# Optimization experiments

Measured on AMD Instinct MI355X. Metric: run time of the kernel, lower is better.

Reference implementation:

```python
import jax, jax.numpy as jnp
import numpy as np

NUM_ITERS = 10
G_KSIZE, G_SIGMA = 5, 0.5
BIL_KSIZE, BIL_SIG_COLOR, BIL_SIG_SPACE = 5, 0.5, 5.0
EDGE_KSIZE, EDGE_SIG_COLOR, EDGE_SIG_SPACE = 5, 0.5, 5.0


def _gauss1d(ksize, sigma):
    x = jnp.arange(ksize, dtype=jnp.float32) - ksize // 2  # odd ksize -> centered (kornia)
    g = jnp.exp(-(x * x) / (2.0 * sigma * sigma))
    return g / g.sum()


def gaussian_blur(q, ksize, sigma):
    # separable gaussian blur with reflect padding, kornia GaussianBlur2d semantics
    k = _gauss1d(ksize, sigma)
    r = ksize // 2
    B, C, H, W = q.shape
    qp = jnp.pad(q, ((0, 0), (0, 0), (r, r), (0, 0)), mode='reflect')
    q = sum(k[i] * qp[:, :, i:i + H, :] for i in range(ksize))
    qp = jnp.pad(q, ((0, 0), (0, 0), (0, 0), (r, r)), mode='reflect')
    q = sum(k[i] * qp[:, :, :, i:i + W] for i in range(ksize))
    return q


def bilateral_weights(guide, ksize, sigma_color, sigma_space):
    # kornia joint_bilateral_blur weights (l1 color distance, reflect border).
    # guide: [B, Cg, H, W] -> weights [B, K*K, H, W]; guidance is constant across
    # CRF iterations so we precompute the kernel once.
    B, Cg, H, W = guide.shape
    r = ksize // 2
    g1 = _gauss1d(ksize, sigma_space)
    space = jnp.outer(g1, g1)  # normalized 2d gaussian (kornia get_gaussian_kernel2d)
    gp = jnp.pad(guide, ((0, 0), (0, 0), (r, r), (r, r)), mode='reflect')
    inv2sc2 = -0.5 / (sigma_color * sigma_color)
    ws = []
    for dy in range(ksize):
        for dx in range(ksize):
            d = jnp.abs(gp[:, :, dy:dy + H, dx:dx + W] - guide).sum(axis=1)  # [B,H,W]
            ws.append(space[dy, dx] * jnp.exp(inv2sc2 * d * d))
    return jnp.stack(ws, axis=1)  # [B, K*K, H, W]


def bilateral_apply(q, weights, ksize):
    # q: [B,C,H,W], weights: [B,K*K,H,W]
    B, C, H, W = q.shape
    r = ksize // 2
    qp = jnp.pad(q, ((0, 0), (0, 0), (r, r), (r, r)), mode='reflect')
    num = jnp.zeros_like(q)
    idx = 0
    for dy in range(ksize):
        for dx in range(ksize):
            num = num + weights[:, idx][:, None] * qp[:, :, dy:dy + H, dx:dx + W]
            idx += 1
    den = weights.sum(axis=1)[:, None]  # [B,1,H,W]
    return num / den


def _compat(f):
    # compat matrix is -1 off-diagonal, 0 on diagonal:
    # pairwise[c] = -sum_{c'!=c} f[c'] = f[c] - sum_{c'} f[c']
    return f - f.sum(axis=1, keepdims=True)


def setup_inputs() -> dict:
    key = jax.random.key(0)
    k1, k2, k3 = jax.random.split(key, 3)
    B, C, H, W = 2, 21, 512, 512
    unary_logits = jax.random.normal(k1, (B, C, H, W), dtype=jnp.float32)
    image = jax.random.uniform(k2, (B, 3, H, W), dtype=jnp.float32)
    edges = jax.random.uniform(k3, (B, H, W), dtype=jnp.float32)
    return {"unary_logits": unary_logits, "image": image, "edges": edges}


def reference(unary_logits, image, edges):
    edges4 = edges[:, None]  # [B,1,H,W]
    w_rgb = bilateral_weights(image, BIL_KSIZE, BIL_SIG_COLOR, BIL_SIG_SPACE)
    w_edge = bilateral_weights(edges4, EDGE_KSIZE, EDGE_SIG_COLOR, EDGE_SIG_SPACE)
    q = jax.nn.softmax(unary_logits, axis=1)
    for _ in range(NUM_ITERS):
        sf = gaussian_blur(q, G_KSIZE, G_SIGMA)
        rf = bilateral_apply(q, w_rgb, BIL_KSIZE)
        ef = bilateral_apply(q, w_edge, EDGE_KSIZE)
        pairwise = _compat(sf) + _compat(rf) + _compat(ef)
        q = jax.nn.softmax(unary_logits - pairwise, axis=1)
    return q
```

## Files before the change

### kernel.cpp

```cpp
#include <hip/hip_runtime.h>
#include <math.h>

#define BATCH 2
#define NCH 21
#define CPAD 24
#define HH 512
#define WW 512
#define KS 5
#define RAD 2
#define NTAPS 25
#define NPAIR 13
#define NUM_ITERS 10

#define TX 32
#define TY 8
#define HX (TX + 2*RAD)
#define HY (TY + 2*RAD)
#define HPX (HX * HY)

typedef _Float16 f16;
typedef _Float16 half8 __attribute__((ext_vector_type(8)));
typedef _Float16 half2v __attribute__((ext_vector_type(2)));

__device__ __forceinline__ int refl(int i, int n) {
    if (i < 0) i = -i;
    if (i >= n) i = 2*n - 2 - i;
    return i;
}

__global__ __launch_bounds__(256) void weights_kernel(const float* __restrict__ image,
                                                      const float* __restrict__ edges,
                                                      half2v* __restrict__ wc2) {
    __shared__ float sr_[HY][HX];
    __shared__ float sg_[HY][HX];
    __shared__ float sb_[HY][HX];
    __shared__ float se_[HY][HX];

    const int tx = threadIdx.x;
    const int ty = threadIdx.y;
    const int tid = ty * TX + tx;
    const int x0 = blockIdx.x * TX;
    const int y0 = blockIdx.y * TY;
    const int b = blockIdx.z;
    const int x = x0 + tx;
    const int y = y0 + ty;
    const size_t plane = (size_t)HH * WW;
    const float* img = image + (size_t)b * 3 * plane;
    const float* edg = edges + (size_t)b * plane;

    for (int i = tid; i < HPX; i += TX * TY) {
        int ly = i / HX, lx = i - ly * HX;
        int gy = refl(y0 + ly - RAD, HH);
        int gx = refl(x0 + lx - RAD, WW);
        int g = gy * WW + gx;
        sr_[ly][lx] = img[g];
        sg_[ly][lx] = img[plane + g];
        sb_[ly][lx] = img[2 * plane + g];
        se_[ly][lx] = edg[g];
    }
    __syncthreads();

    float gs[3];
    gs[0] = 1.0f; gs[1] = __expf(-1.0f / 50.0f); gs[2] = __expf(-4.0f / 50.0f);
    float gb[3];
    gb[0] = 1.0f; gb[1] = __expf(-2.0f); gb[2] = __expf(-8.0f);
    float gbs = gb[0] + 2.0f * (gb[1] + gb[2]);
    gb[0] /= gbs; gb[1] /= gbs; gb[2] /= gbs;

    const float r0 = sr_[ty + RAD][tx + RAD];
    const float g0 = sg_[ty + RAD][tx + RAD];
    const float b0 = sb_[ty + RAD][tx + RAD];
    const float e0 = se_[ty + RAD][tx + RAD];

    float wr[NTAPS], we[NTAPS];
    float sr = 0.f, se = 0.f;
#pragma unroll
    for (int dy = 0; dy < KS; dy++) {
#pragma unroll
        for (int dx = 0; dx < KS; dx++) {
            float sp = gs[abs(dy - RAD)] * gs[abs(dx - RAD)];
            float d = fabsf(sr_[ty + dy][tx + dx] - r0)
                    + fabsf(sg_[ty + dy][tx + dx] - g0)
                    + fabsf(sb_[ty + dy][tx + dx] - b0);
            float w1 = sp * __expf(-2.0f * d * d);
            float de = fabsf(se_[ty + dy][tx + dx] - e0);
            float w2 = sp * __expf(-2.0f * de * de);
            wr[dy * KS + dx] = w1;
            we[dy * KS + dx] = w2;
            sr += w1;
            se += w2;
        }
    }
    float isr = 1.0f / sr, ise = 1.0f / se;
    float wt[NTAPS + 1];
#pragma unroll
    for (int t = 0; t < NTAPS; t++) {
        int dy = t / KS, dx = t % KS;
        float g2 = gb[abs(dy - RAD)] * gb[abs(dx - RAD)];
        wt[t] = g2 + wr[t] * isr + we[t] * ise;
    }
    wt[NTAPS] = 0.f;
#pragma unroll
    for (int p = 0; p < NPAIR; p++) {
        half2v h;
        h[0] = (f16)wt[2 * p];
        h[1] = (f16)wt[2 * p + 1];
        wc2[((size_t)b * NPAIR + p) * plane + (size_t)y * WW + x] = h;
    }
}

__global__ void init_kernel(const float* __restrict__ unary,
                            f16* __restrict__ q,
                            f16* __restrict__ u16) {
    int idx = blockIdx.x * blockDim.x + threadIdx.x;
    if (idx >= BATCH * HH * WW) return;
    int p = idx % (HH * WW);
    int b = idx / (HH * WW);
    const size_t plane = (size_t)HH * WW;
    const float* u = unary + (size_t)b * NCH * plane + p;
    float l[CPAD];
    float m = -1e30f;
#pragma unroll
    for (int c = 0; c < NCH; c++) { l[c] = u[c * plane]; m = fmaxf(m, l[c]); }
    l[21] = 0.f; l[22] = 0.f; l[23] = 0.f;

    half8* uo = (half8*)(u16 + ((size_t)b * plane + p) * CPAD);
#pragma unroll
    for (int g = 0; g < 3; g++) {
        half8 v;
#pragma unroll
        for (int k = 0; k < 8; k++) v[k] = (f16)l[g * 8 + k];
        uo[g] = v;
    }

    float s = 0.f;
    float e[CPAD];
#pragma unroll
    for (int c = 0; c < NCH; c++) { e[c] = __expf(l[c] - m); s += e[c]; }
    float is = 1.0f / s;
    e[21] = 0.f; e[22] = 0.f; e[23] = 0.f;
    half8* qo = (half8*)(q + ((size_t)b * plane + p) * CPAD);
#pragma unroll
    for (int g = 0; g < 3; g++) {
        half8 v;
#pragma unroll
        for (int k = 0; k < 8; k++) v[k] = (f16)(e[g * 8 + k] * is);
        qo[g] = v;
    }
}

template <bool FINAL>
__global__ __launch_bounds__(256, 4) void crf_iter_kernel(const f16* __restrict__ qin,
                                                          const f16* __restrict__ u16,
                                                          const half2v* __restrict__ wc2,
                                                          void* __restrict__ qout) {
    __shared__ __align__(16) f16 tileH[HPX][CPAD];

    const int tx = threadIdx.x;
    const int ty = threadIdx.y;
    const int tid = ty * TX + tx;
    const int x0 = blockIdx.x * TX;
    const int y0 = blockIdx.y * TY;
    const int b = blockIdx.z;
    const int x = x0 + tx;
    const int y = y0 + ty;
    const size_t plane = (size_t)HH * WW;

    const f16* qb = qin + (size_t)b * plane * CPAD;
    for (int idx = tid; idx < HPX * 3; idx += TX * TY) {
        int px = idx / 3, h4 = idx - px * 3;
        int ly = px / HX, lx = px - ly * HX;
        int gy = refl(y0 + ly - RAD, HH);
        int gx = refl(x0 + lx - RAD, WW);
        half8 v = *(const half8*)(qb + ((size_t)gy * WW + gx) * CPAD + h4 * 8);
        *(half8*)&tileH[px][h4 * 8] = v;
    }

    float wcr[NTAPS + 1];
    {
        const half2v* wp = wc2 + (size_t)b * NPAIR * plane + (size_t)y * WW + x;
#pragma unroll
        for (int p = 0; p < NPAIR; p++) {
            half2v h = wp[p * plane];
            wcr[2 * p] = (float)h[0];
            wcr[2 * p + 1] = (float)h[1];
        }
    }

    __syncthreads();

    float acc[NCH];
#pragma unroll
    for (int c = 0; c < NCH; c++) acc[c] = 0.f;

    const int base = ty * HX + tx;
#pragma unroll
    for (int dy = 0; dy < KS; dy++) {
#pragma unroll
        for (int dx = 0; dx < KS; dx++) {
            const float w = wcr[dy * KS + dx];
            const f16* tp = &tileH[base + dy * HX + dx][0];
            half8 v0 = *(const half8*)(tp);
            half8 v1 = *(const half8*)(tp + 8);
            half8 v2 = *(const half8*)(tp + 16);
#pragma unroll
            for (int k = 0; k < 8; k++) acc[k]      = fmaf((float)v0[k], w, acc[k]);
#pragma unroll
            for (int k = 0; k < 8; k++) acc[8 + k]  = fmaf((float)v1[k], w, acc[8 + k]);
#pragma unroll
            for (int k = 0; k < 5; k++) acc[16 + k] = fmaf((float)v2[k], w, acc[16 + k]);
        }
    }

    const f16* ub = u16 + ((size_t)b * plane + (size_t)y * WW + x) * CPAD;
    half8 u0 = *(const half8*)(ub);
    half8 u1 = *(const half8*)(ub + 8);
    half8 u2 = *(const half8*)(ub + 16);
    float l[NCH];
#pragma unroll
    for (int k = 0; k < 8; k++) l[k] = (float)u0[k] - acc[k];
#pragma unroll
    for (int k = 0; k < 8; k++) l[8 + k] = (float)u1[k] - acc[8 + k];
#pragma unroll
    for (int k = 0; k < 5; k++) l[16 + k] = (float)u2[k] - acc[16 + k];

    float m = l[0];
#pragma unroll
    for (int c = 1; c < NCH; c++) m = fmaxf(m, l[c]);
    float s = 0.f;
#pragma unroll
    for (int c = 0; c < NCH; c++) { l[c] = __expf(l[c] - m); s += l[c]; }
    float is = 1.0f / s;
#pragma unroll
    for (int c = 0; c < NCH; c++) l[c] *= is;

    if (FINAL) {
        float* qo = (float*)qout + (size_t)b * NCH * plane + (size_t)y * WW + x;
#pragma unroll
        for (int c = 0; c < NCH; c++) qo[c * plane] = l[c];
    } else {
        half8* qo = (half8*)((f16*)qout + ((size_t)b * plane + (size_t)y * WW + x) * CPAD);
        float lp[CPAD];
#pragma unroll
        for (int c = 0; c < NCH; c++) lp[c] = l[c];
        lp[21] = 0.f; lp[22] = 0.f; lp[23] = 0.f;
#pragma unroll
        for (int g = 0; g < 3; g++) {
            half8 v;
#pragma unroll
            for (int k = 0; k < 8; k++) v[k] = (f16)lp[g * 8 + k];
            qo[g] = v;
        }
    }
}

extern "C" void kernel_launch(void* const* d_in, const int* in_sizes, int n_in,
                              void* d_out, int out_size, void* d_ws, size_t ws_size,
                              hipStream_t stream) {
    const float* unary = (const float*)d_in[0];
    const float* image = (const float*)d_in[1];
    const float* edges = (const float*)d_in[2];
    float* out = (float*)d_out;

    const size_t plane = (size_t)HH * WW;
    char* ws = (char*)d_ws;
    half2v* wc2 = (half2v*)ws;
    char* p1 = ws + sizeof(half2v) * BATCH * NPAIR * plane;
    f16* u16 = (f16*)p1;
    char* p2 = p1 + sizeof(f16) * BATCH * plane * CPAD;
    f16* qA = (f16*)p2;
    f16* qB = qA + (size_t)BATCH * plane * CPAD;

    const int npix = BATCH * HH * WW;
    dim3 grid(WW / TX, HH / TY, BATCH);
    dim3 block(TX, TY, 1);

    weights_kernel<<<grid, block, 0, stream>>>(image, edges, wc2);
    init_kernel<<<(npix + 255) / 256, 256, 0, stream>>>(unary, qA, u16);

    f16* qa = qA;
    f16* qb = qB;
    for (int it = 0; it < NUM_ITERS - 1; it++) {
        crf_iter_kernel<false><<<grid, block, 0, stream>>>(qa, u16, wc2, (void*)qb);
        f16* t = qa; qa = qb; qb = t;
    }
    crf_iter_kernel<true><<<grid, block, 0, stream>>>(qa, u16, wc2, (void*)out);
}
```

Baseline: 338.9 us.

## Load halo tile via direct global-to-LDS loads, remap blocks for L2 locality

Replaces the register-staged halo load with __builtin_amdgcn_global_load_lds so the q tile is copied from global memory straight into LDS, unrolled into fixed rounds. The grid becomes a flat 1D launch with a swizzled block index that groups blocks into row bands, likely to improve L2/MALL reuse of neighbouring halos across XCDs. The unary loads are hoisted before the barrier to overlap with the tile fill, and launch bounds rise to 5 blocks per SM, which adds register pressure. The direct-to-LDS path relies on a contiguous idx*8 layout in LDS that matches tileH, and it needs correct waitcnt handling before the barrier.

Result: faster. 317.3 us (-6.4%).

```diff
diff --git a/kernel.cpp b/kernel.cpp
--- a/kernel.cpp
+++ b/kernel.cpp
@@ -17,6 +17,7 @@
 #define HX (TX + 2*RAD)
 #define HY (TY + 2*RAD)
 #define HPX (HX * HY)
+#define NCHUNK (HPX * 3)
 
 typedef _Float16 f16;
 typedef _Float16 half8 __attribute__((ext_vector_type(8)));
@@ -150,30 +151,53 @@
 }
 
 template <bool FINAL>
-__global__ __launch_bounds__(256, 4) void crf_iter_kernel(const f16* __restrict__ qin,
+__global__ __launch_bounds__(256, 5) void crf_iter_kernel(const f16* __restrict__ qin,
                                                           const f16* __restrict__ u16,
                                                           const half2v* __restrict__ wc2,
                                                           void* __restrict__ qout) {
     __shared__ __align__(16) f16 tileH[HPX][CPAD];
 
-    const int tx = threadIdx.x;
-    const int ty = threadIdx.y;
-    const int tid = ty * TX + tx;
-    const int x0 = blockIdx.x * TX;
-    const int y0 = blockIdx.y * TY;
-    const int b = blockIdx.z;
+    const int tid = threadIdx.x;
+    const int tx = tid & (TX - 1);
+    const int ty = tid >> 5;
+
+    const int flat = blockIdx.x;
+    const int band = flat & 7;
+    const int within = flat >> 3;
+    const int b = within >> 7;
+    const int r = within & 127;
+    const int x0 = (r & 15) * TX;
+    const int y0 = (band * 8 + (r >> 4)) * TY;
     const int x = x0 + tx;
     const int y = y0 + ty;
     const size_t plane = (size_t)HH * WW;
 
     const f16* qb = qin + (size_t)b * plane * CPAD;
-    for (int idx = tid; idx < HPX * 3; idx += TX * TY) {
+    f16* lbase = &tileH[0][0];
+#pragma unroll
+    for (int rnd = 0; rnd < 5; rnd++) {
+        int idx = tid + rnd * 256;
         int px = idx / 3, h4 = idx - px * 3;
         int ly = px / HX, lx = px - ly * HX;
         int gy = refl(y0 + ly - RAD, HH);
         int gx = refl(x0 + lx - RAD, WW);
-        half8 v = *(const half8*)(qb + ((size_t)gy * WW + gx) * CPAD + h4 * 8);
-        *(half8*)&tileH[px][h4 * 8] = v;
+        const f16* g = qb + ((size_t)(gy * WW + gx)) * CPAD + h4 * 8;
+        __builtin_amdgcn_global_load_lds(
+            (const __attribute__((address_space(1))) void*)g,
+            (__attribute__((address_space(3))) void*)(lbase + (size_t)idx * 8),
+            16, 0, 0);
+    }
+    if (tid < NCHUNK - 5 * 256) {
+        int idx = tid + 5 * 256;
+        int px = idx / 3, h4 = idx - px * 3;
+        int ly = px / HX, lx = px - ly * HX;
+        int gy = refl(y0 + ly - RAD, HH);
+        int gx = refl(x0 + lx - RAD, WW);
+        const f16* g = qb + ((size_t)(gy * WW + gx)) * CPAD + h4 * 8;
+        __builtin_amdgcn_global_load_lds(
+            (const __attribute__((address_space(1))) void*)g,
+            (__attribute__((address_space(3))) void*)(lbase + (size_t)idx * 8),
+            16, 0, 0);
     }
 
     float wcr[NTAPS + 1];
@@ -186,6 +210,10 @@
             wcr[2 * p + 1] = (float)h[1];
         }
     }
+    const f16* ub = u16 + ((size_t)b * plane + (size_t)y * WW + x) * CPAD;
+    half8 u0 = *(const half8*)(ub);
+    half8 u1 = *(const half8*)(ub + 8);
+    half8 u2 = *(const half8*)(ub + 16);
 
     __syncthreads();
 
@@ -212,10 +240,6 @@
         }
     }
 
-    const f16* ub = u16 + ((size_t)b * plane + (size_t)y * WW + x) * CPAD;
-    half8 u0 = *(const half8*)(ub);
-    half8 u1 = *(const half8*)(ub + 8);
-    half8 u2 = *(const half8*)(ub + 16);
     float l[NCH];
 #pragma unroll
     for (int k = 0; k < 8; k++) l[k] = (float)u0[k] - acc[k];
@@ -272,17 +296,17 @@
     f16* qB = qA + (size_t)BATCH * plane * CPAD;
 
     const int npix = BATCH * HH * WW;
-    dim3 grid(WW / TX, HH / TY, BATCH);
-    dim3 block(TX, TY, 1);
-
-    weights_kernel<<<grid, block, 0, stream>>>(image, edges, wc2);
+    dim3 gridW(WW / TX, HH / TY, BATCH);
+    dim3 blockW(TX, TY, 1);
+    weights_kernel<<<gridW, blockW, 0, stream>>>(image, edges, wc2);
     init_kernel<<<(npix + 255) / 256, 256, 0, stream>>>(unary, qA, u16);
 
+    const int nblk = (WW / TX) * (HH / TY) * BATCH;
     f16* qa = qA;
     f16* qb = qB;
     for (int it = 0; it < NUM_ITERS - 1; it++) {
-        crf_iter_kernel<false><<<grid, block, 0, stream>>>(qa, u16, wc2, (void*)qb);
+        crf_iter_kernel<false><<<nblk, 256, 0, stream>>>(qa, u16, wc2, (void*)qb);
         f16* t = qa; qa = qb; qb = t;
     }
-    crf_iter_kernel<true><<<grid, block, 0, stream>>>(qa, u16, wc2, (void*)out);
-}
+    crf_iter_kernel<true><<<nblk, 256, 0, stream>>>(qa, u16, wc2, (void*)out);
+}
```

## Compute two pixels per thread with direct-to-LDS loads and pixel-major weights

Applied to the files above, without the earlier changes.

Each thread of the CRF iteration kernel now computes two horizontally adjacent pixels. The six LDS column reads per row are shared across both pixels' 5-tap windows, which cuts LDS traffic per output. The halo tile grows to 32x16 and is filled with global_load_lds, skipping the trip through registers. Filter weights move to a pixel-major layout (24 taps contiguous plus a separate last tap) so they can be read with vector loads. Block indices are remapped into row bands, presumably for L2 locality. The trade-off is double the accumulator registers under launch_bounds(256,4), which risks spilling or lower occupancy.

After: 607.4 us. 79.3% more time.

```diff
diff --git a/kernel.cpp b/kernel.cpp
--- a/kernel.cpp
+++ b/kernel.cpp
@@ -9,14 +9,20 @@
 #define KS 5
 #define RAD 2
 #define NTAPS 25
-#define NPAIR 13
 #define NUM_ITERS 10
 
-#define TX 32
-#define TY 8
-#define HX (TX + 2*RAD)
-#define HY (TY + 2*RAD)
-#define HPX (HX * HY)
+#define TXW 32
+#define TYW 8
+#define HXW (TXW + 2*RAD)
+#define HYW (TYW + 2*RAD)
+#define HPXW (HXW * HYW)
+
+#define TW 32
+#define TH 16
+#define HX2 (TW + 2*RAD)
+#define HY2 (TH + 2*RAD)
+#define HPX2 (HX2 * HY2)
+#define NCHUNK (HPX2 * 3)
 
 typedef _Float16 f16;
 typedef _Float16 half8 __attribute__((ext_vector_type(8)));
@@ -28,19 +34,23 @@
     return i;
 }
 
+#define WSEL(h0, h1, h2, hl, t) \
+    ((t) < 8 ? (h0)[(t)] : (t) < 16 ? (h1)[(t) - 8] : (t) < 24 ? (h2)[(t) - 16] : (hl))
+
 __global__ __launch_bounds__(256) void weights_kernel(const float* __restrict__ image,
                                                       const float* __restrict__ edges,
-                                                      half2v* __restrict__ wc2) {
-    __shared__ float sr_[HY][HX];
-    __shared__ float sg_[HY][HX];
-    __shared__ float sb_[HY][HX];
-    __shared__ float se_[HY][HX];
+                                                      f16* __restrict__ wcA,
+                                                      f16* __restrict__ wcB16) {
+    __shared__ float sr_[HYW][HXW];
+    __shared__ float sg_[HYW][HXW];
+    __shared__ float sb_[HYW][HXW];
+    __shared__ float se_[HYW][HXW];
 
     const int tx = threadIdx.x;
     const int ty = threadIdx.y;
-    const int tid = ty * TX + tx;
-    const int x0 = blockIdx.x * TX;
-    const int y0 = blockIdx.y * TY;
+    const int tid = ty * TXW + tx;
+    const int x0 = blockIdx.x * TXW;
+    const int y0 = blockIdx.y * TYW;
     const int b = blockIdx.z;
     const int x = x0 + tx;
     const int y = y0 + ty;
@@ -48,8 +58,8 @@
     const float* img = image + (size_t)b * 3 * plane;
     const float* edg = edges + (size_t)b * plane;
 
-    for (int i = tid; i < HPX; i += TX * TY) {
-        int ly = i / HX, lx = i - ly * HX;
+    for (int i = tid; i < HPXW; i += TXW * TYW) {
+        int ly = i / HXW, lx = i - ly * HXW;
         int gy = refl(y0 + ly - RAD, HH);
         int gx = refl(x0 + lx - RAD, WW);
         int g = gy * WW + gx;
@@ -92,21 +102,23 @@
         }
     }
     float isr = 1.0f / sr, ise = 1.0f / se;
-    float wt[NTAPS + 1];
+    float wt[NTAPS];
 #pragma unroll
     for (int t = 0; t < NTAPS; t++) {
         int dy = t / KS, dx = t % KS;
         float g2 = gb[abs(dy - RAD)] * gb[abs(dx - RAD)];
         wt[t] = g2 + wr[t] * isr + we[t] * ise;
     }
-    wt[NTAPS] = 0.f;
-#pragma unroll
-    for (int p = 0; p < NPAIR; p++) {
-        half2v h;
-        h[0] = (f16)wt[2 * p];
-        h[1] = (f16)wt[2 * p + 1];
-        wc2[((size_t)b * NPAIR + p) * plane + (size_t)y * WW + x] = h;
-    }
+    const size_t pixoff = (size_t)b * plane + (size_t)y * WW + x;
+    half8* wo = (half8*)(wcA + pixoff * 24);
+#pragma unroll
+    for (int g = 0; g < 3; g++) {
+        half8 v;
+#pragma unroll
+        for (int k = 0; k < 8; k++) v[k] = (f16)wt[g * 8 + k];
+        wo[g] = v;
+    }
+    wcB16[pixoff] = (f16)wt[24];
 }
 
 __global__ void init_kernel(const float* __restrict__ unary,
@@ -152,105 +164,139 @@
 template <bool FINAL>
 __global__ __launch_bounds__(256, 4) void crf_iter_kernel(const f16* __restrict__ qin,
                                                           const f16* __restrict__ u16,
-                                                          const half2v* __restrict__ wc2,
+                                                          const f16* __restrict__ wcA,
+                                                          const f16* __restrict__ wcB16,
                                                           void* __restrict__ qout) {
-    __shared__ __align__(16) f16 tileH[HPX][CPAD];
-
-    const int tx = threadIdx.x;
-    const int ty = threadIdx.y;
-    const int tid = ty * TX + tx;
-    const int x0 = blockIdx.x * TX;
-    const int y0 = blockIdx.y * TY;
-    const int b = blockIdx.z;
-    const int x = x0 + tx;
-    const int y = y0 + ty;
+    __shared__ __align__(16) f16 tileH[HPX2][CPAD];
+
+    const int tid = threadIdx.x;
+    const int txh = tid & 15;
+    const int tyh = tid >> 4;
+
+    const int flat = blockIdx.x;
+    const int band = flat & 7;
+    const int within = flat >> 3;
+    const int b = within >> 6;
+    const int r = within & 63;
+    const int x0 = (r & 15) * TW;
+    const int y0 = (band * 4 + (r >> 4)) * TH;
+    const int x = x0 + txh * 2;
+    const int y = y0 + tyh;
     const size_t plane = (size_t)HH * WW;
 
     const f16* qb = qin + (size_t)b * plane * CPAD;
-    for (int idx = tid; idx < HPX * 3; idx += TX * TY) {
+    f16* lbase = &tileH[0][0];
+    for (int idx = tid; idx < NCHUNK; idx += 256) {
         int px = idx / 3, h4 = idx - px * 3;
-        int ly = px / HX, lx = px - ly * HX;
+        int ly = px / HX2, lx = px - ly * HX2;
         int gy = refl(y0 + ly - RAD, HH);
         int gx = refl(x0 + lx - RAD, WW);
-        half8 v = *(const half8*)(qb + ((size_t)gy * WW + gx) * CPAD + h4 * 8);
-        *(half8*)&tileH[px][h4 * 8] = v;
-    }
-
-    float wcr[NTAPS + 1];
-    {
-        const half2v* wp = wc2 + (size_t)b * NPAIR * plane + (size_t)y * WW + x;
-#pragma unroll
-        for (int p = 0; p < NPAIR; p++) {
-            half2v h = wp[p * plane];
-            wcr[2 * p] = (float)h[0];
-            wcr[2 * p + 1] = (float)h[1];
-        }
-    }
+        const f16* g = qb + ((size_t)(gy * WW + gx)) * CPAD + h4 * 8;
+        __builtin_amdgcn_global_load_lds(
+            (const __attribute__((address_space(1))) void*)g,
+            (__attribute__((address_space(3))) void*)(lbase + (size_t)idx * 8),
+            16, 0, 0);
+    }
+
+    const size_t pixoff = (size_t)b * plane + (size_t)y * WW + x;
+    const half8* wpa = (const half8*)(wcA + pixoff * 24);
+    half8 wa0 = wpa[0], wa1 = wpa[1], wa2 = wpa[2];
+    half8 wb0 = wpa[3], wb1 = wpa[4], wb2 = wpa[5];
+    half2v wl = *(const half2v*)(wcB16 + pixoff);
 
     __syncthreads();
 
-    float acc[NCH];
-#pragma unroll
-    for (int c = 0; c < NCH; c++) acc[c] = 0.f;
-
-    const int base = ty * HX + tx;
+    float acc0[NCH], acc1[NCH];
+#pragma unroll
+    for (int c = 0; c < NCH; c++) { acc0[c] = 0.f; acc1[c] = 0.f; }
+
 #pragma unroll
     for (int dy = 0; dy < KS; dy++) {
-#pragma unroll
-        for (int dx = 0; dx < KS; dx++) {
-            const float w = wcr[dy * KS + dx];
-            const f16* tp = &tileH[base + dy * HX + dx][0];
+        const f16* rowp = &tileH[(tyh + dy) * HX2 + txh * 2][0];
+#pragma unroll
+        for (int j = 0; j < 6; j++) {
+            const f16* tp = rowp + j * CPAD;
             half8 v0 = *(const half8*)(tp);
             half8 v1 = *(const half8*)(tp + 8);
             half8 v2 = *(const half8*)(tp + 16);
-#pragma unroll
-            for (int k = 0; k < 8; k++) acc[k]      = fmaf((float)v0[k], w, acc[k]);
-#pragma unroll
-            for (int k = 0; k < 8; k++) acc[8 + k]  = fmaf((float)v1[k], w, acc[8 + k]);
-#pragma unroll
-            for (int k = 0; k < 5; k++) acc[16 + k] = fmaf((float)v2[k], w, acc[16 + k]);
+            if (j < 5) {
+                const int t = dy * KS + j;
+                const float w = (float)WSEL(wa0, wa1, wa2, wl[0], t);
+#pragma unroll
+                for (int k = 0; k < 8; k++) acc0[k]      = fmaf((float)v0[k], w, acc0[k]);
+#pragma unroll
+                for (int k = 0; k < 8; k++) acc0[8 + k]  = fmaf((float)v1[k], w, acc0[8 + k]);
+#pragma unroll
+                for (int k = 0; k < 5; k++) acc0[16 + k] = fmaf((float)v2[k], w, acc0[16 + k]);
+            }
+            if (j >= 1) {
+                const int t = dy * KS + j - 1;
+                const float w = (float)WSEL(wb0, wb1, wb2, wl[1], t);
+#pragma unroll
+                for (int k = 0; k < 8; k++) acc1[k]      = fmaf((float)v0[k], w, acc1[k]);
+#pragma unroll
+                for (int k = 0; k < 8; k++) acc1[8 + k]  = fmaf((float)v1[k], w, acc1[8 + k]);
+#pragma unroll
+                for (int k = 0; k < 5; k++) acc1[16 + k] = fmaf((float)v2[k], w, acc1[16 + k]);
+            }
         }
     }
 
-    const f16* ub = u16 + ((size_t)b * plane + (size_t)y * WW + x) * CPAD;
-    half8 u0 = *(const half8*)(ub);
-    half8 u1 = *(const half8*)(ub + 8);
-    half8 u2 = *(const half8*)(ub + 16);
-    float l[NCH];
-#pragma unroll
-    for (int k = 0; k < 8; k++) l[k] = (float)u0[k] - acc[k];
-#pragma unroll
-    for (int k = 0; k < 8; k++) l[8 + k] = (float)u1[k] - acc[8 + k];
-#pragma unroll
-    for (int k = 0; k < 5; k++) l[16 + k] = (float)u2[k] - acc[16 + k];
-
-    float m = l[0];
-#pragma unroll
-    for (int c = 1; c < NCH; c++) m = fmaxf(m, l[c]);
-    float s = 0.f;
-#pragma unroll
-    for (int c = 0; c < NCH; c++) { l[c] = __expf(l[c] - m); s += l[c]; }
-    float is = 1.0f / s;
-#pragma unroll
-    for (int c = 0; c < NCH; c++) l[c] *= is;
+    const half8* ub = (const half8*)(u16 + pixoff * CPAD);
+    {
+        half8 u0 = ub[0], u1 = ub[1], u2 = ub[2];
+#pragma unroll
+        for (int k = 0; k < 8; k++) acc0[k] = (float)u0[k] - acc0[k];
+#pragma unroll
+        for (int k = 0; k < 8; k++) acc0[8 + k] = (float)u1[k] - acc0[8 + k];
+#pragma unroll
+        for (int k = 0; k < 5; k++) acc0[16 + k] = (float)u2[k] - acc0[16 + k];
+        u0 = ub[3]; u1 = ub[4]; u2 = ub[5];
+#pragma unroll
+        for (int k = 0; k < 8; k++) acc1[k] = (float)u0[k] - acc1[k];
+#pragma unroll
+        for (int k = 0; k < 8; k++) acc1[8 + k] = (float)u1[k] - acc1[8 + k];
+#pragma unroll
+        for (int k = 0; k < 5; k++) acc1[16 + k] = (float)u2[k] - acc1[16 + k];
+    }
+
+    float m0 = acc0[0], m1 = acc1[0];
+#pragma unroll
+    for (int c = 1; c < NCH; c++) { m0 = fmaxf(m0, acc0[c]); m1 = fmaxf(m1, acc1[c]); }
+    float s0 = 0.f, s1 = 0.f;
+#pragma unroll
+    for (int c = 0; c < NCH; c++) {
+        acc0[c] = __expf(acc0[c] - m0); s0 += acc0[c];
+        acc1[c] = __expf(acc1[c] - m1); s1 += acc1[c];
+    }
+    float is0 = 1.0f / s0, is1 = 1.0f / s1;
 
     if (FINAL) {
         float* qo = (float*)qout + (size_t)b * NCH * plane + (size_t)y * WW + x;
 #pragma unroll
-        for (int c = 0; c < NCH; c++) qo[c * plane] = l[c];
+        for (int c = 0; c < NCH; c++) {
+            float2 v = make_float2(acc0[c] * is0, acc1[c] * is1);
+            *(float2*)(qo + (size_t)c * plane) = v;
+        }
     } else {
-        half8* qo = (half8*)((f16*)qout + ((size_t)b * plane + (size_t)y * WW + x) * CPAD);
-        float lp[CPAD];
-#pragma unroll
-        for (int c = 0; c < NCH; c++) lp[c] = l[c];
-        lp[21] = 0.f; lp[22] = 0.f; lp[23] = 0.f;
-#pragma unroll
-        for (int g = 0; g < 3; g++) {
-            half8 v;
-#pragma unroll
-            for (int k = 0; k < 8; k++) v[k] = (f16)lp[g * 8 + k];
-            qo[g] = v;
-        }
+        half8* qo = (half8*)((f16*)qout + pixoff * CPAD);
+        half8 o0, o1, o2;
+#pragma unroll
+        for (int k = 0; k < 8; k++)  o0[k] = (f16)(acc0[k] * is0);
+#pragma unroll
+        for (int k = 0; k < 8; k++)  o1[k] = (f16)(acc0[8 + k] * is0);
+#pragma unroll
+        for (int k = 0; k < 5; k++)  o2[k] = (f16)(acc0[16 + k] * is0);
+        o2[5] = (f16)0.f; o2[6] = (f16)0.f; o2[7] = (f16)0.f;
+        qo[0] = o0; qo[1] = o1; qo[2] = o2;
+#pragma unroll
+        for (int k = 0; k < 8; k++)  o0[k] = (f16)(acc1[k] * is1);
+#pragma unroll
+        for (int k = 0; k < 8; k++)  o1[k] = (f16)(acc1[8 + k] * is1);
+#pragma unroll
+        for (int k = 0; k < 5; k++)  o2[k] = (f16)(acc1[16 + k] * is1);
+        o2[5] = (f16)0.f; o2[6] = (f16)0.f; o2[7] = (f16)0.f;
+        qo[3] = o0; qo[4] = o1; qo[5] = o2;
     }
 }
 
@@ -264,25 +310,27 @@
 
     const size_t plane = (size_t)HH * WW;
     char* ws = (char*)d_ws;
-    half2v* wc2 = (half2v*)ws;
-    char* p1 = ws + sizeof(half2v) * BATCH * NPAIR * plane;
-    f16* u16 = (f16*)p1;
-    char* p2 = p1 + sizeof(f16) * BATCH * plane * CPAD;
-    f16* qA = (f16*)p2;
+    f16* wcA = (f16*)ws;
+    char* p1 = ws + sizeof(f16) * BATCH * plane * 24;
+    f16* wcB16 = (f16*)p1;
+    char* p2 = p1 + sizeof(f16) * BATCH * plane;
+    f16* u16 = (f16*)p2;
+    char* p3 = p2 + sizeof(f16) * BATCH * plane * CPAD;
+    f16* qA = (f16*)p3;
     f16* qB = qA + (size_t)BATCH * plane * CPAD;
 
     const int npix = BATCH * HH * WW;
-    dim3 grid(WW / TX, HH / TY, BATCH);
-    dim3 block(TX, TY, 1);
-
-    weights_kernel<<<grid, block, 0, stream>>>(image, edges, wc2);
+    dim3 gridW(WW / TXW, HH / TYW, BATCH);
+    dim3 blockW(TXW, TYW, 1);
+    weights_kernel<<<gridW, blockW, 0, stream>>>(image, edges, wcA, wcB16);
     init_kernel<<<(npix + 255) / 256, 256, 0, stream>>>(unary, qA, u16);
 
+    const int nblk = (WW / TW) * (HH / TH) * BATCH;
     f16* qa = qA;
     f16* qb = qB;
     for (int it = 0; it < NUM_ITERS - 1; it++) {
-        crf_iter_kernel<false><<<grid, block, 0, stream>>>(qa, u16, wc2, (void*)qb);
+        crf_iter_kernel<false><<<nblk, 256, 0, stream>>>(qa, u16, wcA, wcB16, (void*)qb);
         f16* t = qa; qa = qb; qb = t;
     }
-    crf_iter_kernel<true><<<grid, block, 0, stream>>>(qa, u16, wc2, (void*)out);
-}
+    crf_iter_kernel<true><<<nblk, 256, 0, stream>>>(qa, u16, wcA, wcB16, (void*)out);
+}
```
